# Kernel optimization log

Hardware: AMD Instinct MI355X
Metric: run time of the kernel (lower is better)

Reference implementation:

```python
import jax, jax.numpy as jnp
import numpy as np

B, U, L, H, M = 4, 16, 128, 768, 256   # docs, utterances/doc, tokens/utt, hidden, mentions/doc
HID = 150                               # Score MLP hidden dim
N_CLUSTERS = 32


def setup_inputs() -> dict:
    key = jax.random.key(0)
    ks = jax.random.split(key, 8)
    hidden = jax.random.normal(ks[0], (B, U, L, H), jnp.float32)

    rng = np.random.default_rng(0)
    span_utt = rng.integers(0, U, (B, M))
    span_start = rng.integers(0, L - 8, (B, M))
    span_end = span_start + rng.integers(1, 9, (B, M))  # span length in [1, 8]

    # coreference labels: label[i, j] = 1 iff j is a true antecedent (j < i, same cluster);
    # if mention i has no antecedent, label[i, i] = 1 (the epsilon / new-entity slot).
    clusters = rng.integers(0, N_CLUSTERS, (B, M))
    same = clusters[:, :, None] == clusters[:, None, :]
    ant = same & np.tril(np.ones((M, M), bool), -1)
    labels = ant.astype(np.float32)
    diag = np.arange(M)
    labels[:, diag, diag] = (~ant.any(-1)).astype(np.float32)

    scale = 0.02
    W1 = jax.random.normal(ks[1], (3 * H, HID), jnp.float32) * scale
    W2 = jax.random.normal(ks[2], (HID, HID), jnp.float32) * scale
    W3 = jax.random.normal(ks[3], (HID, 1), jnp.float32) * scale
    return {
        "hidden": hidden,
        "span_utt": jnp.asarray(span_utt, jnp.int32),
        "span_start": jnp.asarray(span_start, jnp.int32),
        "span_end": jnp.asarray(span_end, jnp.int32),
        "labels": jnp.asarray(labels),
        "W1": W1, "b1": jnp.zeros((HID,), jnp.float32),
        "W2": W2, "b2": jnp.zeros((HID,), jnp.float32),
        "W3": W3, "b3": jnp.zeros((1,), jnp.float32),
    }


def reference(hidden, span_utt, span_start, span_end, labels, W1, b1, W2, b2, W3, b3):
    # ---- span mean-pooling (EntityEncoder, aggr='mean') ----
    pos = jnp.arange(L)
    mask = (pos[None, None, :] >= span_start[..., None]) & (pos[None, None, :] < span_end[..., None])
    w = mask.astype(hidden.dtype) / (span_end - span_start)[..., None].astype(hidden.dtype)  # [B,M,L]
    gathered = jnp.take_along_axis(hidden, span_utt[:, :, None, None], axis=1)  # [B,M,L,H]
    pooled = jnp.einsum('bml,bmlh->bmh', w, gathered)  # [B,M,H]

    # ---- pairwise antecedent scoring (PairScorer / Score MLP, dropout=eval) ----
    ii, jj = np.tril_indices(M, -1)  # static pair indices, P = M(M-1)/2
    # concat(i_g, j_g, i_g*j_g) @ W1  ==  i_g@W1a + j_g@W1b + (i_g*j_g)@W1c
    W1a, W1b, W1c = W1[:H], W1[H:2 * H], W1[2 * H:]
    hi = pooled @ W1a   # [B,M,HID]
    hj = pooled @ W1b   # [B,M,HID]
    prod = pooled[:, ii] * pooled[:, jj]                    # [B,P,H]
    h1 = jax.nn.relu(hi[:, ii] + hj[:, jj] + prod @ W1c + b1)
    h2 = jax.nn.relu(h1 @ W2 + b2)
    s = (h2 @ W3 + b3)[..., 0]  # [B,P]

    # ---- per-mention ragged softmax, padded to [M, M] with -1000 ----
    # row i has logits s_ij for j<i plus epsilon=0 at j=i (diagonal of zeros matrix)
    logits = jnp.zeros((B, M, M), hidden.dtype).at[:, ii, jj].set(s)
    valid = jnp.tril(jnp.ones((M, M), bool))
    probs = jax.nn.softmax(jnp.where(valid, logits, -1e30), axis=-1)
    probs = jnp.where(valid, probs, jnp.asarray(-1000.0, hidden.dtype))

    # ---- compute_loss ----
    eps = 1e-8
    prob_sum = jnp.sum(jnp.clip(probs * labels, eps, 1.0 - eps), axis=-1)  # [B,M]
    loss = -jnp.sum(jnp.log(prob_sum))
    return loss
```

## Files before the change

### kernel.cpp

```cpp
#include <hip/hip_runtime.h>
#include <hip/hip_bf16.h>

#define B_ 4
#define U_ 16
#define L_ 128
#define H_ 768
#define M_ 256
#define HID_ 150

typedef _Float16 half8 __attribute__((ext_vector_type(8)));
typedef _Float16 half4t __attribute__((ext_vector_type(4)));
typedef float floatx4 __attribute__((ext_vector_type(4)));
typedef float floatx16 __attribute__((ext_vector_type(16)));

__global__ __launch_bounds__(256) void prep_kernel(
    const float* __restrict__ W1, const float* __restrict__ W2,
    const float* __restrict__ b2, const float* __restrict__ W3,
    _Float16* __restrict__ W1cs, _Float16* __restrict__ W2s,
    _Float16* __restrict__ W1abs, float2* __restrict__ bw)
{
    int idx = blockIdx.x * 256 + threadIdx.x;
    if (blockIdx.x == 0 && threadIdx.x < 160) {
        int n = threadIdx.x;
        bw[n] = (n < HID_) ? make_float2(b2[n], W3[n]) : make_float2(0.f, 0.f);
    }
    if (idx < 245760) {
        int j = idx & 7, l = (idx >> 3) & 63;
        int t1 = (idx >> 9) % 5, kc = idx / 2560;
        int n = t1 * 32 + (l & 31);
        int k = kc * 16 + ((l >> 5) << 3) + j;
        W1cs[idx] = (n < HID_) ? (_Float16)W1[(size_t)(2 * H_ + k) * HID_ + n]
                               : (_Float16)0.f;
        return;
    }
    idx -= 245760;
    if (idx < 25600) {
        int j = idx & 7, l = (idx >> 3) & 63;
        int t2 = (idx >> 9) % 5, kc = idx / 2560;
        int n = t2 * 32 + (l & 31);
        int k = kc * 16 + ((l >> 5) << 3) + j;
        W2s[idx] = (n < HID_ && k < HID_) ? (_Float16)W2[(size_t)k * HID_ + n]
                                          : (_Float16)0.f;
        return;
    }
    idx -= 25600;
    if (idx < 245760) {
        int j = idx & 7, l = (idx >> 3) & 63;
        int u = (idx >> 9) % 20, kc = idx / 10240;
        int n = u * 16 + (l & 15);
        int k = kc * 32 + ((l >> 4) << 3) + j;
        float v = 0.f;
        if (n < HID_) v = W1[(size_t)k * HID_ + n];
        else if (n >= 160 && n < 160 + HID_) v = W1[(size_t)(H_ + k) * HID_ + (n - 160)];
        W1abs[idx] = (_Float16)v;
    }
}

__global__ __launch_bounds__(256) void pool_hihj_kernel(
    const float* __restrict__ hidden, const int* __restrict__ sutt,
    const int* __restrict__ sstart, const int* __restrict__ send,
    const float* __restrict__ b1, const _Float16* __restrict__ W1abs,
    _Float16* __restrict__ pooledh, float* __restrict__ hiF,
    float* __restrict__ hjT)
{
    __shared__ __align__(16) _Float16 spool[16 * 776];
    const int blk = blockIdx.x;
    const int tid = threadIdx.x;

    {
        const int r  = tid >> 4;
        const int cg = tid & 15;
        const int bm = blk * 16 + r;
        const int b  = bm >> 8;
        const int u  = sutt[bm];
        const int st = sstart[bm];
        const int en = send[bm];
        const float inv = 1.0f / (float)(en - st);
        const float* src = hidden + ((size_t)(b * U_ + u) * L_) * H_ + cg * 48;
        float4 s[12];
        #pragma unroll
        for (int q = 0; q < 12; ++q) s[q] = make_float4(0.f, 0.f, 0.f, 0.f);
        for (int l = st; l < en; ++l) {
            const float* p = src + (size_t)l * H_;
            #pragma unroll
            for (int q = 0; q < 12; ++q) {
                float4 v = *(const float4*)(p + q * 4);
                s[q].x += v.x; s[q].y += v.y; s[q].z += v.z; s[q].w += v.w;
            }
        }
        _Float16* sp = &spool[r * 776 + cg * 48];
        _Float16* gp = pooledh + (size_t)bm * H_ + cg * 48;
        #pragma unroll
        for (int q2 = 0; q2 < 6; ++q2) {
            half8 h;
            float4 a = s[q2 * 2], bv = s[q2 * 2 + 1];
            h[0] = (_Float16)(a.x * inv);  h[1] = (_Float16)(a.y * inv);
            h[2] = (_Float16)(a.z * inv);  h[3] = (_Float16)(a.w * inv);
            h[4] = (_Float16)(bv.x * inv); h[5] = (_Float16)(bv.y * inv);
            h[6] = (_Float16)(bv.z * inv); h[7] = (_Float16)(bv.w * inv);
            *(half8*)(sp + q2 * 8) = h;
            *(half8*)(gp + q2 * 8) = h;
        }
    }
    __syncthreads();

    const int w = tid >> 6, lane = tid & 63;
    const int g = lane >> 4, l15 = lane & 15;
    floatx4 acc[5];
    #pragma unroll
    for (int u5 = 0; u5 < 5; ++u5) acc[u5] = (floatx4){0.f, 0.f, 0.f, 0.f};
    const _Float16* aB = &spool[l15 * 776 + g * 8];
    for (int kc = 0; kc < 24; ++kc) {
        half8 av = *(const half8*)(aB + kc * 32);
        #pragma unroll
        for (int u5 = 0; u5 < 5; ++u5) {
            const int u = w * 5 + u5;
            half8 bv = *(const half8*)(W1abs + (size_t)((kc * 20 + u) * 64 + lane) * 8);
            acc[u5] = __builtin_amdgcn_mfma_f32_16x16x32_f16(av, bv, acc[u5], 0, 0, 0);
        }
    }
    const int row0 = blk * 16 + g * 4;
    #pragma unroll
    for (int u5 = 0; u5 < 5; ++u5) {
        const int n = (w * 5 + u5) * 16 + l15;
        if (n < HID_) {
            float b1v = b1[n];
            #pragma unroll
            for (int r = 0; r < 4; ++r)
                hiF[(size_t)(row0 + r) * 160 + n] = acc[u5][r] + b1v;
        } else if (n >= 160 && n < 160 + HID_) {
            *(float4*)&hjT[(size_t)(n - 160) * 1024 + row0] =
                make_float4(acc[u5][0], acc[u5][1], acc[u5][2], acc[u5][3]);
        }
    }
}

__global__ __launch_bounds__(64, 2) void pair_mlp_kernel(
    const _Float16* __restrict__ pooledh,
    const float* __restrict__ hiF, const float* __restrict__ hjT,
    const _Float16* __restrict__ W1cs, const _Float16* __restrict__ W2s,
    const float2* __restrict__ bw, const float* __restrict__ b3,
    float* __restrict__ logits)
{
    __shared__ __align__(16) _Float16 h1L[2 * 32 * 170];

    int q = blockIdx.x;
    const int b = q / 576;
    int r = q - b * 576;
    int jt = 0;
    while (r >= 128 - 16 * jt) { r -= 128 - 16 * jt; ++jt; }
    const int p = 16 * jt + r;
    const int i0 = 2 * p, j0 = jt * 32;
    const int bm = b * M_;
    const int lane = threadIdx.x & 63;
    const int c31 = lane & 31;
    const int hw = lane >> 5;

    const _Float16* pjp  = pooledh + (size_t)(bm + j0 + c31) * H_ + (hw << 3);
    const _Float16* pip0 = pooledh + (size_t)(bm + i0) * H_ + (hw << 3);
    const _Float16* pip1 = pooledh + (size_t)(bm + i0 + 1) * H_ + (hw << 3);

    floatx16 acc1[2][5];
    #pragma unroll
    for (int t = 0; t < 2; ++t)
        #pragma unroll
        for (int t1 = 0; t1 < 5; ++t1)
            #pragma unroll
            for (int e = 0; e < 16; ++e) acc1[t][t1][e] = 0.f;

    for (int kc = 0; kc < 24; ++kc) {
        half8 pj0 = *(const half8*)(pjp + kc * 32);
        half8 pj1 = *(const half8*)(pjp + kc * 32 + 16);
        #pragma unroll
        for (int h = 0; h < 2; ++h) {
            half8 pj = h ? pj1 : pj0;
            half8 a0 = *(const half8*)((h ? pip0 + 16 : pip0) + kc * 32) * pj;
            half8 a1 = *(const half8*)((h ? pip1 + 16 : pip1) + kc * 32) * pj;
            const _Float16* wbase = W1cs + (size_t)((kc * 2 + h) * 5) * 512 + lane * 8;
            #pragma unroll
            for (int t1 = 0; t1 < 5; ++t1) {
                half8 wf = *(const half8*)(wbase + t1 * 512);
                acc1[0][t1] = __builtin_amdgcn_mfma_f32_32x32x16_f16(
                    wf, a0, acc1[0][t1], 0, 0, 0);
                acc1[1][t1] = __builtin_amdgcn_mfma_f32_32x32x16_f16(
                    wf, a1, acc1[1][t1], 0, 0, 0);
            }
        }
    }

    #pragma unroll
    for (int t1 = 0; t1 < 5; ++t1) {
        #pragma unroll
        for (int qd = 0; qd < 4; ++qd) {
            const int n1 = t1 * 32 + 8 * qd + 4 * hw;
            float hj0 = hjT[(size_t)(n1 + 0) * 1024 + bm + j0 + c31];
            float hj1 = hjT[(size_t)(n1 + 1) * 1024 + bm + j0 + c31];
            float hj2 = hjT[(size_t)(n1 + 2) * 1024 + bm + j0 + c31];
            float hj3 = hjT[(size_t)(n1 + 3) * 1024 + bm + j0 + c31];
            #pragma unroll
            for (int t = 0; t < 2; ++t) {
                float4 hiv = *(const float4*)&hiF[(size_t)(bm + i0 + t) * 160 + n1];
                half4t hv;
                hv[0] = (_Float16)fmaxf(acc1[t][t1][4 * qd + 0] + hiv.x + hj0, 0.f);
                hv[1] = (_Float16)fmaxf(acc1[t][t1][4 * qd + 1] + hiv.y + hj1, 0.f);
                hv[2] = (_Float16)fmaxf(acc1[t][t1][4 * qd + 2] + hiv.z + hj2, 0.f);
                hv[3] = (_Float16)fmaxf(acc1[t][t1][4 * qd + 3] + hiv.w + hj3, 0.f);
                *(half4t*)&h1L[(t * 32 + c31) * 170 + n1] = hv;
            }
        }
    }
    __syncthreads();

    const float b3v = b3[0];
    #pragma unroll
    for (int t = 0; t < 2; ++t) {
        floatx16 acc2[5];
        #pragma unroll
        for (int t2 = 0; t2 < 5; ++t2)
            #pragma unroll
            for (int e = 0; e < 16; ++e) acc2[t2][e] = 0.f;

        for (int kc2 = 0; kc2 < 10; ++kc2) {
            half8 b2f = *(const half8*)&h1L[(t * 32 + c31) * 170 + kc2 * 16 + hw * 8];
            const _Float16* wbase = W2s + (size_t)(kc2 * 5) * 512 + lane * 8;
            #pragma unroll
            for (int t2 = 0; t2 < 5; ++t2) {
                half8 wf = *(const half8*)(wbase + t2 * 512);
                acc2[t2] = __builtin_amdgcn_mfma_f32_32x32x16_f16(
                    wf, b2f, acc2[t2], 0, 0, 0);
            }
        }

        float sown = 0.f;
        #pragma unroll
        for (int t2 = 0; t2 < 5; ++t2) {
            #pragma unroll
            for (int qd = 0; qd < 4; ++qd) {
                const int n2 = t2 * 32 + 8 * qd + 4 * hw;
                float4 bw01 = *(const float4*)&bw[n2];
                float4 bw23 = *(const float4*)&bw[n2 + 2];
                sown += fmaxf(acc2[t2][4 * qd + 0] + bw01.x, 0.f) * bw01.y;
                sown += fmaxf(acc2[t2][4 * qd + 1] + bw01.z, 0.f) * bw01.w;
                sown += fmaxf(acc2[t2][4 * qd + 2] + bw23.x, 0.f) * bw23.y;
                sown += fmaxf(acc2[t2][4 * qd + 3] + bw23.z, 0.f) * bw23.w;
            }
        }
        float s = sown + __shfl_xor(sown, 32);
        const int i = i0 + t;
        const int j = j0 + c31;
        if (lane < 32 && j < i)
            logits[(size_t)(bm + i) * M_ + j] = s + b3v;
    }
}

__global__ __launch_bounds__(256) void loss_kernel(
    const float* __restrict__ logits, const float* __restrict__ labels,
    float* __restrict__ out)
{
    const int bm = blockIdx.x;
    const int i  = bm & (M_ - 1);
    const int j  = threadIdx.x;
    __shared__ float red[4];
    __shared__ float bcast;

    float val = (j < i) ? logits[(size_t)bm * M_ + j]
                        : ((j == i) ? 0.0f : -1e30f);

    float m = val;
    #pragma unroll
    for (int off = 32; off >= 1; off >>= 1) m = fmaxf(m, __shfl_down(m, off, 64));
    const int wave = j >> 6, lane = j & 63;
    if (lane == 0) red[wave] = m;
    __syncthreads();
    if (j == 0) bcast = fmaxf(fmaxf(red[0], red[1]), fmaxf(red[2], red[3]));
    __syncthreads();
    const float mm = bcast;

    float e = (j <= i) ? expf(val - mm) : 0.0f;
    float s = e;
    #pragma unroll
    for (int off = 32; off >= 1; off >>= 1) s += __shfl_down(s, off, 64);
    __syncthreads();
    if (lane == 0) red[wave] = s;
    __syncthreads();
    if (j == 0) bcast = red[0] + red[1] + red[2] + red[3];
    __syncthreads();
    const float ssum = bcast;

    float prob = (j <= i) ? (e / ssum) : -1000.0f;
    float lab = labels[(size_t)bm * M_ + j];
    float tv = prob * lab;
    tv = fminf(fmaxf(tv, 1e-8f), 1.0f - 1e-8f);
    float rs = tv;
    #pragma unroll
    for (int off = 32; off >= 1; off >>= 1) rs += __shfl_down(rs, off, 64);
    __syncthreads();
    if (lane == 0) red[wave] = rs;
    __syncthreads();
    if (j == 0) atomicAdd(out, -logf(red[0] + red[1] + red[2] + red[3]));
}

extern "C" void kernel_launch(void* const* d_in, const int* in_sizes, int n_in,
                              void* d_out, int out_size, void* d_ws, size_t ws_size,
                              hipStream_t stream)
{
    const float* hidden = (const float*)d_in[0];
    const int*   sutt   = (const int*)d_in[1];
    const int*   sstart = (const int*)d_in[2];
    const int*   send   = (const int*)d_in[3];
    const float* labels = (const float*)d_in[4];
    const float* W1     = (const float*)d_in[5];
    const float* b1     = (const float*)d_in[6];
    const float* W2     = (const float*)d_in[7];
    const float* b2     = (const float*)d_in[8];
    const float* W3     = (const float*)d_in[9];
    const float* b3     = (const float*)d_in[10];

    float* ws = (float*)d_ws;
    float*    hiF     = ws;
    float*    hjT     = ws + 163840;
    float*    logits  = ws + 327680;
    float2*   bw      = (float2*)(ws + 589824);
    _Float16* pooledh = (_Float16*)(ws + 590144);
    _Float16* W1cs    = (_Float16*)(ws + 983360);
    _Float16* W2s     = (_Float16*)(ws + 1106240);
    _Float16* W1abs   = (_Float16*)(ws + 1119040);
    float* out = (float*)d_out;

    hipMemsetAsync(d_out, 0, sizeof(float), stream);

    prep_kernel<<<dim3(2020), 256, 0, stream>>>(W1, W2, b2, W3,
                                                W1cs, W2s, W1abs, bw);
    pool_hihj_kernel<<<dim3(64), 256, 0, stream>>>(hidden, sutt, sstart, send,
                                                   b1, W1abs, pooledh, hiF, hjT);
    pair_mlp_kernel<<<dim3(576 * B_), 64, 0, stream>>>(pooledh, hiF, hjT,
                                                       W1cs, W2s, bw, b3, logits);
    loss_kernel<<<dim3(B_ * M_), 256, 0, stream>>>(logits, labels, out);
}
```

Baseline: 214.3 us.

## Stage W1c tiles in shared memory across four waves; split pooling kernel

The pair MLP kernel now runs four waves per block, and the W1c weight slices are double-buffered in LDS and shared by four i-pairs instead of each wave streaming them from global memory. Span pooling moves into its own kernel with more blocks, and the hi/hj GEMM reads the pooled rows back from global memory. The prep kernel is reindexed so its reads of W1 and W2 are coalesced rather than its writes. These trade fewer redundant weight loads and more parallelism in pooling for an extra launch, per-chunk barriers, and more LDS per block.

```diff
diff --git a/kernel.cpp b/kernel.cpp
--- a/kernel.cpp
+++ b/kernel.cpp
@@ -24,83 +24,78 @@
         int n = threadIdx.x;
         bw[n] = (n < HID_) ? make_float2(b2[n], W3[n]) : make_float2(0.f, 0.f);
     }
-    if (idx < 245760) {
-        int j = idx & 7, l = (idx >> 3) & 63;
-        int t1 = (idx >> 9) % 5, kc = idx / 2560;
-        int n = t1 * 32 + (l & 31);
-        int k = kc * 16 + ((l >> 5) << 3) + j;
-        W1cs[idx] = (n < HID_) ? (_Float16)W1[(size_t)(2 * H_ + k) * HID_ + n]
-                               : (_Float16)0.f;
+    if (idx < 122880) {
+        int k = idx / 160, n = idx - k * 160;
+        float v = (n < HID_) ? W1[(size_t)(2 * H_ + k) * HID_ + n] : 0.f;
+        W1cs[(k >> 4) * 2560 + (n >> 5) * 512 +
+             (((n & 31) | (((k >> 3) & 1) << 5)) << 3) + (k & 7)] = (_Float16)v;
         return;
     }
-    idx -= 245760;
+    idx -= 122880;
     if (idx < 25600) {
-        int j = idx & 7, l = (idx >> 3) & 63;
-        int t2 = (idx >> 9) % 5, kc = idx / 2560;
-        int n = t2 * 32 + (l & 31);
-        int k = kc * 16 + ((l >> 5) << 3) + j;
-        W2s[idx] = (n < HID_ && k < HID_) ? (_Float16)W2[(size_t)k * HID_ + n]
-                                          : (_Float16)0.f;
+        int k = idx / 160, n = idx - k * 160;
+        float v = (k < HID_ && n < HID_) ? W2[(size_t)k * HID_ + n] : 0.f;
+        W2s[(k >> 4) * 2560 + (n >> 5) * 512 +
+            (((n & 31) | (((k >> 3) & 1) << 5)) << 3) + (k & 7)] = (_Float16)v;
         return;
     }
     idx -= 25600;
     if (idx < 245760) {
-        int j = idx & 7, l = (idx >> 3) & 63;
-        int u = (idx >> 9) % 20, kc = idx / 10240;
-        int n = u * 16 + (l & 15);
-        int k = kc * 32 + ((l >> 4) << 3) + j;
+        int k = idx / 320, n = idx - k * 320;
         float v = 0.f;
         if (n < HID_) v = W1[(size_t)k * HID_ + n];
         else if (n >= 160 && n < 160 + HID_) v = W1[(size_t)(H_ + k) * HID_ + (n - 160)];
-        W1abs[idx] = (_Float16)v;
-    }
-}
-
-__global__ __launch_bounds__(256) void pool_hihj_kernel(
+        W1abs[(k >> 5) * 10240 + (n >> 4) * 512 +
+              (((n & 15) | (((k >> 3) & 3) << 4)) << 3) + (k & 7)] = (_Float16)v;
+    }
+}
+
+__global__ __launch_bounds__(256) void pool_kernel(
     const float* __restrict__ hidden, const int* __restrict__ sutt,
     const int* __restrict__ sstart, const int* __restrict__ send,
-    const float* __restrict__ b1, const _Float16* __restrict__ W1abs,
-    _Float16* __restrict__ pooledh, float* __restrict__ hiF,
-    float* __restrict__ hjT)
+    _Float16* __restrict__ pooledh)
+{
+    const int bm = blockIdx.x * 4 + (threadIdx.x >> 6);
+    const int lane = threadIdx.x & 63;
+    const int b  = bm >> 8;
+    const int u  = sutt[bm];
+    const int st = sstart[bm];
+    const int en = send[bm];
+    const float inv = 1.0f / (float)(en - st);
+    const float* src = hidden + ((size_t)(b * U_ + u) * L_) * H_ + lane * 12;
+    float4 s[3];
+    #pragma unroll
+    for (int q = 0; q < 3; ++q) s[q] = make_float4(0.f, 0.f, 0.f, 0.f);
+    for (int l = st; l < en; ++l) {
+        const float* p = src + (size_t)l * H_;
+        #pragma unroll
+        for (int q = 0; q < 3; ++q) {
+            float4 v = *(const float4*)(p + q * 4);
+            s[q].x += v.x; s[q].y += v.y; s[q].z += v.z; s[q].w += v.w;
+        }
+    }
+    _Float16* gp = pooledh + (size_t)bm * H_ + lane * 12;
+    #pragma unroll
+    for (int q = 0; q < 3; ++q) {
+        half4t hv;
+        hv[0] = (_Float16)(s[q].x * inv); hv[1] = (_Float16)(s[q].y * inv);
+        hv[2] = (_Float16)(s[q].z * inv); hv[3] = (_Float16)(s[q].w * inv);
+        *(half4t*)(gp + q * 4) = hv;
+    }
+}
+
+__global__ __launch_bounds__(256) void hihj_kernel(
+    const _Float16* __restrict__ pooledh, const float* __restrict__ b1,
+    const _Float16* __restrict__ W1abs,
+    float* __restrict__ hiF, float* __restrict__ hjT)
 {
     __shared__ __align__(16) _Float16 spool[16 * 776];
     const int blk = blockIdx.x;
     const int tid = threadIdx.x;
-
-    {
-        const int r  = tid >> 4;
-        const int cg = tid & 15;
-        const int bm = blk * 16 + r;
-        const int b  = bm >> 8;
-        const int u  = sutt[bm];
-        const int st = sstart[bm];
-        const int en = send[bm];
-        const float inv = 1.0f / (float)(en - st);
-        const float* src = hidden + ((size_t)(b * U_ + u) * L_) * H_ + cg * 48;
-        float4 s[12];
-        #pragma unroll
-        for (int q = 0; q < 12; ++q) s[q] = make_float4(0.f, 0.f, 0.f, 0.f);
-        for (int l = st; l < en; ++l) {
-            const float* p = src + (size_t)l * H_;
-            #pragma unroll
-            for (int q = 0; q < 12; ++q) {
-                float4 v = *(const float4*)(p + q * 4);
-                s[q].x += v.x; s[q].y += v.y; s[q].z += v.z; s[q].w += v.w;
-            }
-        }
-        _Float16* sp = &spool[r * 776 + cg * 48];
-        _Float16* gp = pooledh + (size_t)bm * H_ + cg * 48;
-        #pragma unroll
-        for (int q2 = 0; q2 < 6; ++q2) {
-            half8 h;
-            float4 a = s[q2 * 2], bv = s[q2 * 2 + 1];
-            h[0] = (_Float16)(a.x * inv);  h[1] = (_Float16)(a.y * inv);
-            h[2] = (_Float16)(a.z * inv);  h[3] = (_Float16)(a.w * inv);
-            h[4] = (_Float16)(bv.x * inv); h[5] = (_Float16)(bv.y * inv);
-            h[6] = (_Float16)(bv.z * inv); h[7] = (_Float16)(bv.w * inv);
-            *(half8*)(sp + q2 * 8) = h;
-            *(half8*)(gp + q2 * 8) = h;
-        }
+    for (int e = tid; e < 16 * 96; e += 256) {
+        int r = e / 96, c = e - r * 96;
+        *(half8*)&spool[r * 776 + c * 8] =
+            *(const half8*)&pooledh[(size_t)(blk * 16 + r) * H_ + c * 8];
     }
     __syncthreads();
 
@@ -135,26 +130,26 @@
     }
 }
 
-__global__ __launch_bounds__(64, 2) void pair_mlp_kernel(
+__global__ __launch_bounds__(256, 2) void pair_mlp_kernel(
     const _Float16* __restrict__ pooledh,
     const float* __restrict__ hiF, const float* __restrict__ hjT,
     const _Float16* __restrict__ W1cs, const _Float16* __restrict__ W2s,
     const float2* __restrict__ bw, const float* __restrict__ b3,
     float* __restrict__ logits)
 {
-    __shared__ __align__(16) _Float16 h1L[2 * 32 * 170];
-
-    int q = blockIdx.x;
-    const int b = q / 576;
-    int r = q - b * 576;
+    __shared__ __align__(16) _Float16 sW[2][5120];
+    __shared__ __align__(16) _Float16 h1L[4][5440];
+
+    const int b = blockIdx.y;
+    int t = blockIdx.x;
     int jt = 0;
-    while (r >= 128 - 16 * jt) { r -= 128 - 16 * jt; ++jt; }
-    const int p = 16 * jt + r;
-    const int i0 = 2 * p, j0 = jt * 32;
+    while (t >= 32 - 4 * jt) { t -= 32 - 4 * jt; ++jt; }
+    const int tid = threadIdx.x;
+    const int w = tid >> 6, lane = tid & 63;
+    const int p = 16 * jt + 4 * t + w;
+    const int i0 = 2 * p, j0 = 32 * jt;
     const int bm = b * M_;
-    const int lane = threadIdx.x & 63;
-    const int c31 = lane & 31;
-    const int hw = lane >> 5;
+    const int c31 = lane & 31, hw = lane >> 5;
 
     const _Float16* pjp  = pooledh + (size_t)(bm + j0 + c31) * H_ + (hw << 3);
     const _Float16* pip0 = pooledh + (size_t)(bm + i0) * H_ + (hw << 3);
@@ -162,75 +157,95 @@
 
     floatx16 acc1[2][5];
     #pragma unroll
-    for (int t = 0; t < 2; ++t)
+    for (int tt = 0; tt < 2; ++tt)
         #pragma unroll
         for (int t1 = 0; t1 < 5; ++t1)
             #pragma unroll
-            for (int e = 0; e < 16; ++e) acc1[t][t1][e] = 0.f;
+            for (int e = 0; e < 16; ++e) acc1[tt][t1][e] = 0.f;
+
+    half8 s0 = *(const half8*)(W1cs + (size_t)tid * 8);
+    half8 s1 = *(const half8*)(W1cs + (size_t)(tid + 256) * 8);
+    half8 s2;
+    if (tid < 128) s2 = *(const half8*)(W1cs + (size_t)(tid + 512) * 8);
+    *(half8*)&sW[0][tid * 8] = s0;
+    *(half8*)&sW[0][(tid + 256) * 8] = s1;
+    if (tid < 128) *(half8*)&sW[0][(tid + 512) * 8] = s2;
+    __syncthreads();
 
     for (int kc = 0; kc < 24; ++kc) {
-        half8 pj0 = *(const half8*)(pjp + kc * 32);
-        half8 pj1 = *(const half8*)(pjp + kc * 32 + 16);
+        const int pp = kc & 1;
+        if (kc < 23) {
+            const _Float16* g = W1cs + (size_t)(kc + 1) * 5120;
+            s0 = *(const half8*)(g + (size_t)tid * 8);
+            s1 = *(const half8*)(g + (size_t)(tid + 256) * 8);
+            if (tid < 128) s2 = *(const half8*)(g + (size_t)(tid + 512) * 8);
+        }
+        half8 pj0  = *(const half8*)(pjp + kc * 32);
+        half8 pj1  = *(const half8*)(pjp + kc * 32 + 16);
+        half8 pi00 = *(const half8*)(pip0 + kc * 32);
+        half8 pi01 = *(const half8*)(pip0 + kc * 32 + 16);
+        half8 pi10 = *(const half8*)(pip1 + kc * 32);
+        half8 pi11 = *(const half8*)(pip1 + kc * 32 + 16);
         #pragma unroll
         for (int h = 0; h < 2; ++h) {
             half8 pj = h ? pj1 : pj0;
-            half8 a0 = *(const half8*)((h ? pip0 + 16 : pip0) + kc * 32) * pj;
-            half8 a1 = *(const half8*)((h ? pip1 + 16 : pip1) + kc * 32) * pj;
-            const _Float16* wbase = W1cs + (size_t)((kc * 2 + h) * 5) * 512 + lane * 8;
+            half8 a0 = (h ? pi01 : pi00) * pj;
+            half8 a1 = (h ? pi11 : pi10) * pj;
+            const _Float16* base = &sW[pp][h * 2560 + lane * 8];
             #pragma unroll
             for (int t1 = 0; t1 < 5; ++t1) {
-                half8 wf = *(const half8*)(wbase + t1 * 512);
+                half8 wf = *(const half8*)(base + t1 * 512);
                 acc1[0][t1] = __builtin_amdgcn_mfma_f32_32x32x16_f16(
                     wf, a0, acc1[0][t1], 0, 0, 0);
                 acc1[1][t1] = __builtin_amdgcn_mfma_f32_32x32x16_f16(
                     wf, a1, acc1[1][t1], 0, 0, 0);
             }
         }
-    }
-
-    #pragma unroll
-    for (int t1 = 0; t1 < 5; ++t1) {
-        #pragma unroll
-        for (int qd = 0; qd < 4; ++qd) {
-            const int n1 = t1 * 32 + 8 * qd + 4 * hw;
-            float hj0 = hjT[(size_t)(n1 + 0) * 1024 + bm + j0 + c31];
-            float hj1 = hjT[(size_t)(n1 + 1) * 1024 + bm + j0 + c31];
-            float hj2 = hjT[(size_t)(n1 + 2) * 1024 + bm + j0 + c31];
-            float hj3 = hjT[(size_t)(n1 + 3) * 1024 + bm + j0 + c31];
-            #pragma unroll
-            for (int t = 0; t < 2; ++t) {
-                float4 hiv = *(const float4*)&hiF[(size_t)(bm + i0 + t) * 160 + n1];
+        if (kc < 23) {
+            *(half8*)&sW[1 - pp][tid * 8] = s0;
+            *(half8*)&sW[1 - pp][(tid + 256) * 8] = s1;
+            if (tid < 128) *(half8*)&sW[1 - pp][(tid + 512) * 8] = s2;
+            __syncthreads();
+        }
+    }
+
+    const float b3v = b3[0];
+    _Float16* h1w = h1L[w];
+    #pragma unroll
+    for (int tt = 0; tt < 2; ++tt) {
+        #pragma unroll
+        for (int t1 = 0; t1 < 5; ++t1) {
+            #pragma unroll
+            for (int qd = 0; qd < 4; ++qd) {
+                const int n1 = t1 * 32 + 8 * qd + 4 * hw;
+                float hj0 = hjT[(size_t)(n1 + 0) * 1024 + bm + j0 + c31];
+                float hj1 = hjT[(size_t)(n1 + 1) * 1024 + bm + j0 + c31];
+                float hj2 = hjT[(size_t)(n1 + 2) * 1024 + bm + j0 + c31];
+                float hj3 = hjT[(size_t)(n1 + 3) * 1024 + bm + j0 + c31];
+                float4 hiv = *(const float4*)&hiF[(size_t)(bm + i0 + tt) * 160 + n1];
                 half4t hv;
-                hv[0] = (_Float16)fmaxf(acc1[t][t1][4 * qd + 0] + hiv.x + hj0, 0.f);
-                hv[1] = (_Float16)fmaxf(acc1[t][t1][4 * qd + 1] + hiv.y + hj1, 0.f);
-                hv[2] = (_Float16)fmaxf(acc1[t][t1][4 * qd + 2] + hiv.z + hj2, 0.f);
-                hv[3] = (_Float16)fmaxf(acc1[t][t1][4 * qd + 3] + hiv.w + hj3, 0.f);
-                *(half4t*)&h1L[(t * 32 + c31) * 170 + n1] = hv;
+                hv[0] = (_Float16)fmaxf(acc1[tt][t1][4 * qd + 0] + hiv.x + hj0, 0.f);
+                hv[1] = (_Float16)fmaxf(acc1[tt][t1][4 * qd + 1] + hiv.y + hj1, 0.f);
+                hv[2] = (_Float16)fmaxf(acc1[tt][t1][4 * qd + 2] + hiv.z + hj2, 0.f);
+                hv[3] = (_Float16)fmaxf(acc1[tt][t1][4 * qd + 3] + hiv.w + hj3, 0.f);
+                *(half4t*)&h1w[c31 * 170 + n1] = hv;
             }
         }
-    }
-    __syncthreads();
-
-    const float b3v = b3[0];
-    #pragma unroll
-    for (int t = 0; t < 2; ++t) {
         floatx16 acc2[5];
         #pragma unroll
         for (int t2 = 0; t2 < 5; ++t2)
             #pragma unroll
             for (int e = 0; e < 16; ++e) acc2[t2][e] = 0.f;
-
         for (int kc2 = 0; kc2 < 10; ++kc2) {
-            half8 b2f = *(const half8*)&h1L[(t * 32 + c31) * 170 + kc2 * 16 + hw * 8];
-            const _Float16* wbase = W2s + (size_t)(kc2 * 5) * 512 + lane * 8;
+            half8 b2f = *(const half8*)&h1w[c31 * 170 + kc2 * 16 + hw * 8];
+            const _Float16* wb = W2s + (size_t)(kc2 * 5) * 512 + lane * 8;
             #pragma unroll
             for (int t2 = 0; t2 < 5; ++t2) {
-                half8 wf = *(const half8*)(wbase + t2 * 512);
+                half8 wf = *(const half8*)(wb + t2 * 512);
                 acc2[t2] = __builtin_amdgcn_mfma_f32_32x32x16_f16(
                     wf, b2f, acc2[t2], 0, 0, 0);
             }
         }
-
         float sown = 0.f;
         #pragma unroll
         for (int t2 = 0; t2 < 5; ++t2) {
@@ -246,7 +261,7 @@
             }
         }
         float s = sown + __shfl_xor(sown, 32);
-        const int i = i0 + t;
+        const int i = i0 + tt;
         const int j = j0 + c31;
         if (lane < 32 && j < i)
             logits[(size_t)(bm + i) * M_ + j] = s + b3v;
@@ -329,11 +344,11 @@
 
     hipMemsetAsync(d_out, 0, sizeof(float), stream);
 
-    prep_kernel<<<dim3(2020), 256, 0, stream>>>(W1, W2, b2, W3,
+    prep_kernel<<<dim3(1540), 256, 0, stream>>>(W1, W2, b2, W3,
                                                 W1cs, W2s, W1abs, bw);
-    pool_hihj_kernel<<<dim3(64), 256, 0, stream>>>(hidden, sutt, sstart, send,
-                                                   b1, W1abs, pooledh, hiF, hjT);
-    pair_mlp_kernel<<<dim3(576 * B_), 64, 0, stream>>>(pooledh, hiF, hjT,
+    pool_kernel<<<dim3(256), 256, 0, stream>>>(hidden, sutt, sstart, send, pooledh);
+    hihj_kernel<<<dim3(64), 256, 0, stream>>>(pooledh, b1, W1abs, hiF, hjT);
+    pair_mlp_kernel<<<dim3(144, B_), 256, 0, stream>>>(pooledh, hiF, hjT,
                                                        W1cs, W2s, bw, b3, logits);
     loss_kernel<<<dim3(B_ * M_), 256, 0, stream>>>(logits, labels, out);
 }
```

Result: slower. 268.3 us (+25.2%).
